# Performance work log

Hardware: AMD Instinct MI355X
Metric: run time of the kernel (lower is better)

The kernel has to match this reference:

```python
import jax, jax.numpy as jnp
from jax import lax
import numpy as np

N_QUBITS = 10  # min(dim, n_wires) wires carry RX gates; rest stay |0>


def setup_inputs() -> dict:
    key = jax.random.key(0)
    k1, k2, k3, k4 = jax.random.split(key, 4)
    T, B, D, H, C = 128, 512, 512, 512, 32
    inputs = jax.random.normal(k1, (T, B, D), dtype=jnp.float32)
    # 4 gates (f, i, g, o), centres init ~ 0.1 * randn as in the module
    centres = 0.1 * jax.random.normal(k2, (4, C, D + H), dtype=jnp.float32)
    lin_w = jax.random.normal(k3, (4, H, C), dtype=jnp.float32) / jnp.sqrt(jnp.float32(C))
    lin_b = jax.random.normal(k4, (4, H), dtype=jnp.float32) * 0.01
    return {"inputs": inputs, "centres": centres, "lin_w": lin_w, "lin_b": lin_b}


def _quantum_kernel(comb, ctr):
    # comb: [B, dim], ctr: [C, dim]
    # Circuit = RX(x_i) then RX(-y_i) on wire i (i < N_QUBITS) => RX(x_i - y_i).
    # |<0..0|state>| = prod_i |cos((x_i - y_i)/2)| over active wires.
    m = min(comb.shape[-1], N_QUBITS)
    diff = comb[:, None, :m] - ctr[None, :, :m]  # [B, C, m]
    return jnp.prod(jnp.abs(jnp.cos(0.5 * diff)), axis=-1)  # [B, C]


def reference(inputs, centres, lin_w, lin_b):
    T, B, D = inputs.shape
    H = lin_w.shape[1]
    h0 = jnp.zeros((B, H), dtype=inputs.dtype)
    c0 = jnp.zeros((B, H), dtype=inputs.dtype)

    def step(carry, x):
        h, c = carry
        comb = jnp.concatenate([x, h], axis=1)  # [B, D+H]
        # kernels for all 4 gates at once: [4, B, C]
        k = jax.vmap(lambda ct: _quantum_kernel(comb, ct))(centres)
        pre = jnp.einsum('gbc,ghc->gbh', k, lin_w) + lin_b[:, None, :]  # [4, B, H]
        f = jax.nn.sigmoid(pre[0])
        i = jax.nn.sigmoid(pre[1])
        g = jnp.tanh(pre[2])
        o = jax.nn.sigmoid(pre[3])
        c_new = f * c + i * g
        h_new = o * jnp.tanh(c_new)
        return (h_new, c_new), h_new

    (h, c), outputs = lax.scan(step, (h0, c0), inputs)
    return outputs, h, c
```

## Files before the change

kernel.cpp:

```cpp
#include <hip/hip_runtime.h>

#define TT 128
#define BB 512
#define DD 512
#define HH 512
#define CC 32
#define NQ 10
#define GC 128
#define DH 1024
#define CHUNK 8
#define NCHUNK (TT / CHUNK)
#define HLOC 256
#define L2E 1.4426950408889634f
#define KB_PER_B 32768

typedef __fp16 h2 __attribute__((ext_vector_type(2)));
typedef __fp16 h4 __attribute__((ext_vector_type(4)));
typedef __fp16 h8 __attribute__((ext_vector_type(8)));
typedef float f4 __attribute__((ext_vector_type(4)));

__device__ __forceinline__ float rcpf(float x) { return __builtin_amdgcn_rcpf(x); }
__device__ __forceinline__ float exp2fast(float x) {
#if __has_builtin(__builtin_amdgcn_exp2f)
    return __builtin_amdgcn_exp2f(x);
#else
    return exp2f(x);
#endif
}

__global__ __launch_bounds__(256) void qk_kernel(
    const float* __restrict__ inputs,
    const float* __restrict__ centres,
    __fp16* __restrict__ kbuf)
{
    __shared__ float xsA[64 * 12];
    __shared__ float csT[NQ * 128];

    const int bid = blockIdx.x;
    const int b = bid >> 1, th = bid & 1;
    const int tid = threadIdx.x;

    for (int idx = tid; idx < 64 * NQ; idx += 256) {
        int tl = idx / NQ, d = idx - tl * NQ;
        xsA[tl * 12 + d] = 0.5f * inputs[((size_t)(th * 64 + tl) * BB + b) * DD + d];
    }
    for (int idx = tid; idx < GC * NQ; idx += 256) {
        int gc = idx & 127, d = idx >> 7;
        csT[d * 128 + gc] = 0.5f * centres[(size_t)gc * DH + d];
    }
    __syncthreads();

    const int gcq = (tid & 31) * 4;
    const int t0 = tid >> 5;
    char* kb = (char*)kbuf + (size_t)b * KB_PER_B;
    #pragma unroll
    for (int p = 0; p < 8; ++p) {
        const int tl = t0 + p * 8;
        const int t = th * 64 + tl;
        float pr0 = 1.f, pr1 = 1.f, pr2 = 1.f, pr3 = 1.f;
        #pragma unroll
        for (int d = 0; d < NQ; ++d) {
            float xd = xsA[tl * 12 + d];
            f4 cd = *(const f4*)&csT[d * 128 + gcq];
            pr0 *= fabsf(__cosf(xd - cd.x));
            pr1 *= fabsf(__cosf(xd - cd.y));
            pr2 *= fabsf(__cosf(xd - cd.z));
            pr3 *= fabsf(__cosf(xd - cd.w));
        }
        h2 lo2 = __builtin_amdgcn_cvt_pkrtz(pr0, pr1);
        h2 hi2 = __builtin_amdgcn_cvt_pkrtz(pr2, pr3);
        h4 kk = { lo2.x, lo2.y, hi2.x, hi2.y };
        int byteo = (t * 256 + gcq * 2) ^ ((t & 7) << 4);
        *(h4*)(kb + byteo) = kk;
    }
}

__global__ __launch_bounds__(256, 3) void lstm_kernel(
    const __fp16* __restrict__ kbuf,
    const float* __restrict__ lin_w,
    const float* __restrict__ lin_b,
    float* __restrict__ out)
{
    __shared__ __fp16 Klds[TT * GC];
    __shared__ __align__(16) unsigned preBx[CHUNK * HLOC * 2];
    __shared__ float blds[4 * HLOC];

    const int bid = blockIdx.x;
    const int b = bid >> 1;
    const int hbase = (bid & 1) * HLOC;

    const int tid = threadIdx.x;
    const int lane = tid & 63;
    const int w = tid >> 6;
    const int q = lane >> 4;
    const int c16 = lane & 15;
    const int hi = lane >> 5;

    {
        const char* src = (const char*)kbuf + (size_t)b * KB_PER_B;
        #pragma unroll
        for (int half = 0; half < 2; ++half) {
            uint4 t0_ = *(const uint4*)(src + (((half * 4 + 0) * 256 + tid) * 16));
            uint4 t1_ = *(const uint4*)(src + (((half * 4 + 1) * 256 + tid) * 16));
            uint4 t2_ = *(const uint4*)(src + (((half * 4 + 2) * 256 + tid) * 16));
            uint4 t3_ = *(const uint4*)(src + (((half * 4 + 3) * 256 + tid) * 16));
            *(uint4*)((char*)Klds + (((half * 4 + 0) * 256 + tid) * 16)) = t0_;
            *(uint4*)((char*)Klds + (((half * 4 + 1) * 256 + tid) * 16)) = t1_;
            *(uint4*)((char*)Klds + (((half * 4 + 2) * 256 + tid) * 16)) = t2_;
            *(uint4*)((char*)Klds + (((half * 4 + 3) * 256 + tid) * 16)) = t3_;
        }
    }

    for (int idx = tid; idx < 4 * HLOC; idx += 256) {
        int g = idx >> 8, hl = idx & 255;
        float s = (g == 2) ? (2.f * L2E) : (-L2E);
        blds[idx] = s * lin_b[g * HH + hbase + hl];
    }

    h8 bfr[16];
    {
        const int c0 = q * 8;
        #pragma unroll
        for (int g = 0; g < 4; ++g) {
            const float s = (g == 2) ? (2.f * L2E) : (-L2E);
            #pragma unroll
            for (int j = 0; j < 4; ++j) {
                const int hcolg = hbase + w * 64 + j * 16 + c16;
                const float* wp = lin_w + (((size_t)g * HH + hcolg) * CC + c0);
                f4 lo = *(const f4*)wp;
                f4 hif = *(const f4*)(wp + 4);
                h2 p0 = __builtin_amdgcn_cvt_pkrtz(s * lo.x, s * lo.y);
                h2 p1 = __builtin_amdgcn_cvt_pkrtz(s * lo.z, s * lo.w);
                h2 p2 = __builtin_amdgcn_cvt_pkrtz(s * hif.x, s * hif.y);
                h2 p3 = __builtin_amdgcn_cvt_pkrtz(s * hif.z, s * hif.w);
                h8 bb = { p0.x, p0.y, p1.x, p1.y, p2.x, p2.y, p3.x, p3.y };
                bfr[g * 4 + j] = bb;
            }
        }
    }
    __syncthreads();

    float cs2 = 0.f, hstate = 0.f;
    float* op = out + (size_t)b * HH + hbase + tid;
    const int tlo = c16 & 7;
    int aoff[4];
    #pragma unroll
    for (int g = 0; g < 4; ++g)
        aoff[g] = tlo * 256 + ((g * 64 + q * 16) ^ (tlo << 4));
    const int hclbase = w * 64 + c16;
    const int rl0 = (q & 1) * 4;

    for (int ct = 0; ct < NCHUNK; ++ct) {
        const char* arp = (const char*)Klds + ct * 2048;
        h8 afr[4];
        #pragma unroll
        for (int g = 0; g < 4; ++g)
            afr[g] = *(const h8*)(arp + aoff[g]);

        #pragma unroll
        for (int j = 0; j < 4; ++j) {
            const int hcl = hclbase + j * 16;
            const float bf = blds[0 * HLOC + hcl];
            const float bi = blds[1 * HLOC + hcl];
            const float bg = blds[2 * HLOC + hcl];
            const float bo = blds[3 * HLOC + hcl];
            f4 cf = { bf, bf, bf, bf };
            f4 ci = { bi, bi, bi, bi };
            f4 cg = { bg, bg, bg, bg };
            f4 co = { bo, bo, bo, bo };
            f4 aF = __builtin_amdgcn_mfma_f32_16x16x32_f16(afr[0], bfr[0*4+j], cf, 0, 0, 0);
            f4 aI = __builtin_amdgcn_mfma_f32_16x16x32_f16(afr[1], bfr[1*4+j], ci, 0, 0, 0);
            f4 aG = __builtin_amdgcn_mfma_f32_16x16x32_f16(afr[2], bfr[2*4+j], cg, 0, 0, 0);
            f4 aO = __builtin_amdgcn_mfma_f32_16x16x32_f16(afr[3], bfr[3*4+j], co, 0, 0, 0);
            #pragma unroll
            for (int r = 0; r < 4; ++r) {
                float selA = hi ? aI[r] : aF[r];
                float selB = hi ? aG[r] : aO[r];
                float e1 = rcpf(1.f + exp2fast(selA));
                float e2 = rcpf(1.f + exp2fast(selB));
                float gg2 = fmaf(-4.f * L2E, e2, 2.f * L2E);
                float ig2 = e1 * gg2;
                h2 pk = __builtin_amdgcn_cvt_pkrtz(e1, e2);
                unsigned uval = hi ? __builtin_bit_cast(unsigned, ig2)
                                   : *(unsigned*)&pk;
                preBx[((rl0 + r) * HLOC + hcl) * 2 + hi] = uval;
            }
        }

        #pragma unroll
        for (int s = 0; s < CHUNK; ++s) {
            uint2 vv = *(const uint2*)&preBx[(s * HLOC + tid) * 2];
            h2 fo = *(h2*)&vv.x;
            float F = (float)fo.x;
            float O = (float)fo.y;
            float IG2 = __builtin_bit_cast(float, vv.y);
            cs2 = fmaf(F, cs2, IG2);
            float th = fmaf(-2.f, rcpf(1.f + exp2fast(cs2)), 1.f);
            hstate = O * th;
            op[(size_t)(ct * CHUNK + s) * (BB * HH)] = hstate;
        }
    }

    float* hout = out + (size_t)TT * BB * HH;
    float* cout = hout + (size_t)BB * HH;
    hout[(size_t)b * HH + hbase + tid] = hstate;
    cout[(size_t)b * HH + hbase + tid] = cs2 * 0.34657359027997264f;
}

extern "C" void kernel_launch(void* const* d_in, const int* in_sizes, int n_in,
                              void* d_out, int out_size, void* d_ws, size_t ws_size,
                              hipStream_t stream) {
    const float* inputs  = (const float*)d_in[0];
    const float* centres = (const float*)d_in[1];
    const float* lin_w   = (const float*)d_in[2];
    const float* lin_b   = (const float*)d_in[3];
    float* out = (float*)d_out;

    const size_t KBYTES = (size_t)BB * KB_PER_B;
    void* kbuf = (ws_size >= KBYTES)
               ? d_ws
               : (void*)((char*)d_out + (size_t)112 * BB * HH * sizeof(float));

    qk_kernel<<<dim3(1024), dim3(256), 0, stream>>>(inputs, centres, (__fp16*)kbuf);
    lstm_kernel<<<dim3(1024), dim3(256), 0, stream>>>((const __fp16*)kbuf, lin_w, lin_b, out);
}
```

Before: 99.20 us.

## Stream kernel-buffer fragments from global memory instead of staging in LDS

The LSTM kernel stops copying the whole per-batch kernel buffer (32 KB) and bias into shared memory. A-fragments are now loaded directly from global memory with a one-chunk-ahead prefetch, and bias values sit in registers and are added after the MFMA instead of serving as the accumulator init. The smaller LDS footprint allows raising launch bounds to 4 blocks per CU, and block-to-batch mapping changes so the two H-halves of a batch land in different launch waves. The XOR swizzle on the buffer layout is dropped, and the cost moves to global/L2 load latency inside the recurrent loop.

```diff
diff --git a/kernel.cpp b/kernel.cpp
--- a/kernel.cpp
+++ b/kernel.cpp
@@ -12,7 +12,7 @@
 #define NCHUNK (TT / CHUNK)
 #define HLOC 256
 #define L2E 1.4426950408889634f
-#define KB_PER_B 32768
+#define K_ELEMS_PER_B (TT * GC)
 
 typedef __fp16 h2 __attribute__((ext_vector_type(2)));
 typedef __fp16 h4 __attribute__((ext_vector_type(4)));
@@ -52,7 +52,7 @@
 
     const int gcq = (tid & 31) * 4;
     const int t0 = tid >> 5;
-    char* kb = (char*)kbuf + (size_t)b * KB_PER_B;
+    __fp16* kb = kbuf + (size_t)b * K_ELEMS_PER_B;
     #pragma unroll
     for (int p = 0; p < 8; ++p) {
         const int tl = t0 + p * 8;
@@ -70,24 +70,21 @@
         h2 lo2 = __builtin_amdgcn_cvt_pkrtz(pr0, pr1);
         h2 hi2 = __builtin_amdgcn_cvt_pkrtz(pr2, pr3);
         h4 kk = { lo2.x, lo2.y, hi2.x, hi2.y };
-        int byteo = (t * 256 + gcq * 2) ^ ((t & 7) << 4);
-        *(h4*)(kb + byteo) = kk;
-    }
-}
-
-__global__ __launch_bounds__(256, 3) void lstm_kernel(
+        *(h4*)(kb + t * GC + gcq) = kk;
+    }
+}
+
+__global__ __launch_bounds__(256, 4) void lstm_kernel(
     const __fp16* __restrict__ kbuf,
     const float* __restrict__ lin_w,
     const float* __restrict__ lin_b,
     float* __restrict__ out)
 {
-    __shared__ __fp16 Klds[TT * GC];
     __shared__ __align__(16) unsigned preBx[CHUNK * HLOC * 2];
-    __shared__ float blds[4 * HLOC];
 
     const int bid = blockIdx.x;
-    const int b = bid >> 1;
-    const int hbase = (bid & 1) * HLOC;
+    const int b = bid & 511;
+    const int hbase = (bid >> 9) * HLOC;
 
     const int tid = threadIdx.x;
     const int lane = tid & 63;
@@ -96,28 +93,8 @@
     const int c16 = lane & 15;
     const int hi = lane >> 5;
 
-    {
-        const char* src = (const char*)kbuf + (size_t)b * KB_PER_B;
-        #pragma unroll
-        for (int half = 0; half < 2; ++half) {
-            uint4 t0_ = *(const uint4*)(src + (((half * 4 + 0) * 256 + tid) * 16));
-            uint4 t1_ = *(const uint4*)(src + (((half * 4 + 1) * 256 + tid) * 16));
-            uint4 t2_ = *(const uint4*)(src + (((half * 4 + 2) * 256 + tid) * 16));
-            uint4 t3_ = *(const uint4*)(src + (((half * 4 + 3) * 256 + tid) * 16));
-            *(uint4*)((char*)Klds + (((half * 4 + 0) * 256 + tid) * 16)) = t0_;
-            *(uint4*)((char*)Klds + (((half * 4 + 1) * 256 + tid) * 16)) = t1_;
-            *(uint4*)((char*)Klds + (((half * 4 + 2) * 256 + tid) * 16)) = t2_;
-            *(uint4*)((char*)Klds + (((half * 4 + 3) * 256 + tid) * 16)) = t3_;
-        }
-    }
-
-    for (int idx = tid; idx < 4 * HLOC; idx += 256) {
-        int g = idx >> 8, hl = idx & 255;
-        float s = (g == 2) ? (2.f * L2E) : (-L2E);
-        blds[idx] = s * lin_b[g * HH + hbase + hl];
-    }
-
     h8 bfr[16];
+    float bA[4], bB[4];
     {
         const int c0 = q * 8;
         #pragma unroll
@@ -137,45 +114,43 @@
                 bfr[g * 4 + j] = bb;
             }
         }
-    }
-    __syncthreads();
+        #pragma unroll
+        for (int j = 0; j < 4; ++j) {
+            const int hcolg = hbase + w * 64 + j * 16 + c16;
+            float bf_ = -L2E * lin_b[0 * HH + hcolg];
+            float bi_ = -L2E * lin_b[1 * HH + hcolg];
+            float bg_ = 2.f * L2E * lin_b[2 * HH + hcolg];
+            float bo_ = -L2E * lin_b[3 * HH + hcolg];
+            bA[j] = hi ? bi_ : bf_;
+            bB[j] = hi ? bg_ : bo_;
+        }
+    }
 
     float cs2 = 0.f, hstate = 0.f;
     float* op = out + (size_t)b * HH + hbase + tid;
     const int tlo = c16 & 7;
-    int aoff[4];
+    const __fp16* kb = kbuf + (size_t)b * K_ELEMS_PER_B + tlo * GC + q * 8;
+    const int hclbase = w * 64 + c16;
+    const int rl0 = (q & 1) * 4;
+
+    h8 afr[4];
     #pragma unroll
     for (int g = 0; g < 4; ++g)
-        aoff[g] = tlo * 256 + ((g * 64 + q * 16) ^ (tlo << 4));
-    const int hclbase = w * 64 + c16;
-    const int rl0 = (q & 1) * 4;
+        afr[g] = *(const h8*)(kb + g * 32);
 
     for (int ct = 0; ct < NCHUNK; ++ct) {
-        const char* arp = (const char*)Klds + ct * 2048;
-        h8 afr[4];
-        #pragma unroll
-        for (int g = 0; g < 4; ++g)
-            afr[g] = *(const h8*)(arp + aoff[g]);
-
         #pragma unroll
         for (int j = 0; j < 4; ++j) {
             const int hcl = hclbase + j * 16;
-            const float bf = blds[0 * HLOC + hcl];
-            const float bi = blds[1 * HLOC + hcl];
-            const float bg = blds[2 * HLOC + hcl];
-            const float bo = blds[3 * HLOC + hcl];
-            f4 cf = { bf, bf, bf, bf };
-            f4 ci = { bi, bi, bi, bi };
-            f4 cg = { bg, bg, bg, bg };
-            f4 co = { bo, bo, bo, bo };
-            f4 aF = __builtin_amdgcn_mfma_f32_16x16x32_f16(afr[0], bfr[0*4+j], cf, 0, 0, 0);
-            f4 aI = __builtin_amdgcn_mfma_f32_16x16x32_f16(afr[1], bfr[1*4+j], ci, 0, 0, 0);
-            f4 aG = __builtin_amdgcn_mfma_f32_16x16x32_f16(afr[2], bfr[2*4+j], cg, 0, 0, 0);
-            f4 aO = __builtin_amdgcn_mfma_f32_16x16x32_f16(afr[3], bfr[3*4+j], co, 0, 0, 0);
+            const f4 z4 = {0.f, 0.f, 0.f, 0.f};
+            f4 aF = __builtin_amdgcn_mfma_f32_16x16x32_f16(afr[0], bfr[0*4+j], z4, 0, 0, 0);
+            f4 aI = __builtin_amdgcn_mfma_f32_16x16x32_f16(afr[1], bfr[1*4+j], z4, 0, 0, 0);
+            f4 aG = __builtin_amdgcn_mfma_f32_16x16x32_f16(afr[2], bfr[2*4+j], z4, 0, 0, 0);
+            f4 aO = __builtin_amdgcn_mfma_f32_16x16x32_f16(afr[3], bfr[3*4+j], z4, 0, 0, 0);
             #pragma unroll
             for (int r = 0; r < 4; ++r) {
-                float selA = hi ? aI[r] : aF[r];
-                float selB = hi ? aG[r] : aO[r];
+                float selA = (hi ? aI[r] : aF[r]) + bA[j];
+                float selB = (hi ? aG[r] : aO[r]) + bB[j];
                 float e1 = rcpf(1.f + exp2fast(selA));
                 float e2 = rcpf(1.f + exp2fast(selB));
                 float gg2 = fmaf(-4.f * L2E, e2, 2.f * L2E);
@@ -185,6 +160,13 @@
                                    : *(unsigned*)&pk;
                 preBx[((rl0 + r) * HLOC + hcl) * 2 + hi] = uval;
             }
+        }
+
+        if (ct + 1 < NCHUNK) {
+            const __fp16* kn = kb + (ct + 1) * (CHUNK * GC);
+            #pragma unroll
+            for (int g = 0; g < 4; ++g)
+                afr[g] = *(const h8*)(kn + g * 32);
         }
 
         #pragma unroll
@@ -216,7 +198,7 @@
     const float* lin_b   = (const float*)d_in[3];
     float* out = (float*)d_out;
 
-    const size_t KBYTES = (size_t)BB * KB_PER_B;
+    const size_t KBYTES = (size_t)BB * K_ELEMS_PER_B * sizeof(__fp16);
     void* kbuf = (ws_size >= KBYTES)
                ? d_ws
                : (void*)((char*)d_out + (size_t)112 * BB * HH * sizeof(float));
```

Result: faster. 93.92 us (-5.3%).
